# Performance work log

Measured on AMD Instinct MI355X. Metric: run time of the kernel, lower is better.

The kernel has to match this reference:

```python
import jax, jax.numpy as jnp
import numpy as np

N = 100000      # nodes
E = 1600000     # edges (avg degree 16)
F_IN = 128      # dataset.num_features
H = 64          # hidden_channels
C = 40          # dataset.num_classes
LAYERS = 4      # number_conv_layers
EPS = 1e-12     # F.normalize eps


def _agnn_layer(x, src, dst):
    # AGNNConv with beta=1 (requires_grad=False):
    # alpha_ij = softmax_i( cos(x_i, x_j) ), out_i = sum_j alpha_ij * x_j
    xn = x / jnp.maximum(jnp.linalg.norm(x, axis=1, keepdims=True), EPS)
    logits = jnp.sum(xn[dst] * xn[src], axis=1)                      # [E]
    m = jax.lax.stop_gradient(jax.ops.segment_max(logits, dst, num_segments=N))
    e = jnp.exp(logits - m[dst])
    s = jax.ops.segment_sum(e, dst, num_segments=N)
    alpha = e / s[dst]                                               # [E]
    return jax.ops.segment_sum(alpha[:, None] * x[src], dst, num_segments=N)


def setup_inputs() -> dict:
    key = jax.random.key(0)
    k = jax.random.split(key, 6)
    x = jax.random.normal(k[0], (N, F_IN), dtype=jnp.float32)
    edge_index = jax.random.randint(k[1], (2, E), 0, N, dtype=jnp.int32)
    W1 = jax.random.normal(k[2], (F_IN, H), dtype=jnp.float32) * (1.0 / np.sqrt(F_IN))
    b1 = jnp.zeros((H,), dtype=jnp.float32)
    W2 = jax.random.normal(k[3], (H, C), dtype=jnp.float32) * (1.0 / np.sqrt(H))
    b2 = jnp.zeros((C,), dtype=jnp.float32)
    return {"x": x, "W1": W1, "b1": b1, "W2": W2, "b2": b2, "edge_index": edge_index}


def reference(x, W1, b1, W2, b2, edge_index):
    # add self loops (PyG AGNNConv default)
    loop = jnp.arange(N, dtype=edge_index.dtype)
    src = jnp.concatenate([edge_index[0], loop])
    dst = jnp.concatenate([edge_index[1], loop])
    h = jax.nn.relu(x @ W1 + b1)          # lin1 + relu (dropout p=0 / eval)
    for _ in range(LAYERS):
        h = _agnn_layer(h, src, dst)
    out = h @ W2 + b2                     # lin2
    return jax.nn.log_softmax(out, axis=1)
```

## Files before the change

kernel.cpp:

```cpp
#include <hip/hip_runtime.h>
#include <math.h>

#define F_IN 128
#define H_DIM 64
#define C_OUT 40
#define NBK 391
#define CHUNK 4096
#define XPAD 136
#define PHB 128

typedef _Float16 h8 __attribute__((ext_vector_type(8)));
typedef _Float16 half2t __attribute__((ext_vector_type(2)));
typedef float nf4 __attribute__((ext_vector_type(4)));
typedef _Float16 f16x8 __attribute__((ext_vector_type(8)));
typedef float f32x4 __attribute__((ext_vector_type(4)));

union H8 {
    h8 v;
    half2t p[4];
};

__device__ __forceinline__ float dot8(const H8& a, const H8& b) {
    float d = __builtin_amdgcn_fdot2(a.p[0], b.p[0], 0.0f, false);
    d = __builtin_amdgcn_fdot2(a.p[1], b.p[1], d, false);
    d = __builtin_amdgcn_fdot2(a.p[2], b.p[2], d, false);
    d = __builtin_amdgcn_fdot2(a.p[3], b.p[3], d, false);
    return d;
}

__device__ __forceinline__ float dpp_red8_add(float x) {
    int v = __builtin_bit_cast(int, x);
    x += __builtin_bit_cast(float, __builtin_amdgcn_update_dpp(0, v, 0xB1, 0xF, 0xF, true));
    v = __builtin_bit_cast(int, x);
    x += __builtin_bit_cast(float, __builtin_amdgcn_update_dpp(0, v, 0x4E, 0xF, 0xF, true));
    v = __builtin_bit_cast(int, x);
    x += __builtin_bit_cast(float, __builtin_amdgcn_update_dpp(0, v, 0x141, 0xF, 0xF, true));
    return x;
}


__global__ void __launch_bounds__(256) bphist_kernel(const int* __restrict__ dst,
                                                     int* __restrict__ part, int E) {
    __shared__ int lh[512];
    int tid = threadIdx.x;
    lh[tid] = 0; lh[tid + 256] = 0;
    __syncthreads();
    int slice = (E + PHB - 1) / PHB;
    int lo = blockIdx.x * slice;
    int hi = min(E, lo + slice);
    for (int e = lo + tid; e < hi; e += 256) {
        int d = __builtin_nontemporal_load(&dst[e]);
        atomicAdd(&lh[d >> 8], 1);
    }
    __syncthreads();
    part[blockIdx.x * 512 + tid] = lh[tid];
    part[blockIdx.x * 512 + tid + 256] = lh[tid + 256];
}

__global__ void __launch_bounds__(512) bscan_kernel(const int* __restrict__ part,
                                                    int* __restrict__ bbase,
                                                    int* __restrict__ bcursor, int E) {
    __shared__ int sa[512], sb[512];
    int t = threadIdx.x;
    int v = 0;
#pragma unroll 4
    for (int b = 0; b < PHB; b++) v += part[b * 512 + t];
    sa[t] = v;
    __syncthreads();
    int* pa = sa; int* pb = sb;
#pragma unroll
    for (int off = 1; off < 512; off <<= 1) {
        pb[t] = pa[t] + ((t >= off) ? pa[t - off] : 0);
        __syncthreads();
        int* tmp = pa; pa = pb; pb = tmp;
    }
    if (t < NBK) {
        int excl = pa[t] - v;
        bbase[t] = excl;
        bcursor[t] = excl;
    }
    if (t == 0) bbase[NBK] = E;
}

__global__ void __launch_bounds__(256) binscatter_kernel(const int* __restrict__ src,
                                                         const int* __restrict__ dst,
                                                         int* __restrict__ bcursor,
                                                         unsigned int* __restrict__ pairs, int E) {
    __shared__ unsigned int sp[CHUNK];
    __shared__ unsigned short sbof[CHUNK];
    __shared__ int hist[512];
    __shared__ int scanA[512], scanB[512];
    __shared__ int cur[512];
    __shared__ int gbase[512];
    int tid = threadIdx.x;
    int e0 = blockIdx.x * CHUNK;
    int cnt = min(CHUNK, E - e0);

    int dv[CHUNK / 256], sv[CHUNK / 256];
#pragma unroll
    for (int i = 0; i < CHUNK / 256; i++) {
        int idx = tid + i * 256;
        if (idx < cnt) {
            dv[i] = __builtin_nontemporal_load(&dst[e0 + idx]);
            sv[i] = __builtin_nontemporal_load(&src[e0 + idx]);
        }
    }
    hist[tid] = 0; hist[tid + 256] = 0;
    __syncthreads();
#pragma unroll
    for (int i = 0; i < CHUNK / 256; i++) {
        int idx = tid + i * 256;
        if (idx < cnt) atomicAdd(&hist[dv[i] >> 8], 1);
    }
    __syncthreads();
    scanA[tid] = hist[tid]; scanA[tid + 256] = hist[tid + 256];
    __syncthreads();
    int* pa = scanA; int* pb = scanB;
#pragma unroll
    for (int off = 1; off < 512; off <<= 1) {
        pb[tid] = pa[tid] + ((tid >= off) ? pa[tid - off] : 0);
        int t1 = tid + 256;
        pb[t1] = pa[t1] + ((t1 >= off) ? pa[t1 - off] : 0);
        __syncthreads();
        int* tmp = pa; pa = pb; pb = tmp;
    }
    cur[tid] = pa[tid] - hist[tid];
    cur[tid + 256] = pa[tid + 256] - hist[tid + 256];
    __syncthreads();
#pragma unroll
    for (int i = 0; i < CHUNK / 256; i++) {
        int idx = tid + i * 256;
        if (idx < cnt) {
            int b = dv[i] >> 8;
            int lp = atomicAdd(&cur[b], 1);
            sp[lp] = ((unsigned int)(dv[i] & 255) << 24) | (unsigned int)sv[i];
            sbof[lp] = (unsigned short)b;
        }
    }
    {
        int c0 = hist[tid];
        gbase[tid] = c0 ? atomicAdd(&bcursor[tid], c0) : 0;
        int c1 = hist[tid + 256];
        gbase[tid + 256] = c1 ? atomicAdd(&bcursor[tid + 256], c1) : 0;
    }
    __syncthreads();
    for (int i = tid; i < cnt; i += 256) {
        int b = sbof[i];
        int off_in_b = i - (pa[b] - hist[b]);
        pairs[gbase[b] + off_in_b] = sp[i];
    }
}

__global__ void __launch_bounds__(256) bucketsort_kernel(const unsigned int* __restrict__ pairs,
                                                         const int* __restrict__ bbase,
                                                         int* __restrict__ rowptr,
                                                         int* __restrict__ ssrc, int N, int E) {
    __shared__ int hist[256], scanA[256], scanB[256], cur[256];
    int b = blockIdx.x;
    int tid = threadIdx.x;
    int e0 = bbase[b], e1 = bbase[b + 1];
    hist[tid] = 0;
    __syncthreads();
    for (int e = e0 + tid; e < e1; e += 256) {
        unsigned int p = pairs[e];
        atomicAdd(&hist[p >> 24], 1);
    }
    __syncthreads();
    scanA[tid] = hist[tid];
    __syncthreads();
    int* pa = scanA; int* pb = scanB;
#pragma unroll
    for (int off = 1; off < 256; off <<= 1) {
        pb[tid] = pa[tid] + ((tid >= off) ? pa[tid - off] : 0);
        __syncthreads();
        int* tmp = pa; pa = pb; pb = tmp;
    }
    int excl = pa[tid] - hist[tid];
    int node = (b << 8) + tid;
    if (node < N) rowptr[node] = e0 + excl;
    if (b == NBK - 1 && tid == 0) rowptr[N] = E;
    cur[tid] = e0 + excl;
    __syncthreads();
    for (int e = e0 + tid; e < e1; e += 256) {
        unsigned int p = pairs[e];
        int pos = atomicAdd(&cur[p >> 24], 1);
        ssrc[pos] = (int)(p & 0x00FFFFFFu);
    }
}

__global__ void __launch_bounds__(256) cvtw_kernel(const float* __restrict__ W1,
                                                   _Float16* __restrict__ w1t) {
    int t = blockIdx.x * 256 + threadIdx.x;
    if (t < F_IN * H_DIM) {
        int k = t >> 6, col = t & 63;
        w1t[col * F_IN + k] = (_Float16)W1[t];
    }
}

__global__ void __launch_bounds__(256) lin1_kernel(
        const float* __restrict__ x, const _Float16* __restrict__ w1t,
        const float* __restrict__ b1, _Float16* __restrict__ hnout,
        float* __restrict__ nrmout, int n) {
    __shared__ _Float16 sx[64 * XPAD];
    __shared__ _Float16 sw[64 * XPAD];
    int tid = threadIdx.x;
    int r0 = blockIdx.x * 64;

    for (int ch = tid; ch < 64 * 32; ch += 256) {
        int row = ch >> 5, k4 = (ch & 31) << 2;
        float4 xv = make_float4(0.f, 0.f, 0.f, 0.f);
        if (r0 + row < n) xv = *(const float4*)(x + (size_t)(r0 + row) * F_IN + k4);
        _Float16* p = &sx[row * XPAD + k4];
        p[0] = (_Float16)xv.x; p[1] = (_Float16)xv.y;
        p[2] = (_Float16)xv.z; p[3] = (_Float16)xv.w;
    }
    for (int ch = tid; ch < 64 * 16; ch += 256) {
        int col = ch >> 4, k8 = (ch & 15) << 3;
        *(uint4*)&sw[col * XPAD + k8] = *(const uint4*)(w1t + col * F_IN + k8);
    }
    __syncthreads();

    int w = tid >> 6, lane = tid & 63;
    int q = lane >> 4, c = lane & 15;

    f16x8 afrag[4];
#pragma unroll
    for (int kk = 0; kk < 4; kk++)
        afrag[kk] = *(const f16x8*)&sx[(w * 16 + c) * XPAD + kk * 32 + q * 8];

    f32x4 acc[4] = {{0.f,0.f,0.f,0.f},{0.f,0.f,0.f,0.f},{0.f,0.f,0.f,0.f},{0.f,0.f,0.f,0.f}};
#pragma unroll
    for (int ct = 0; ct < 4; ct++) {
#pragma unroll
        for (int kk = 0; kk < 4; kk++) {
            f16x8 bfrag = *(const f16x8*)&sw[(ct * 16 + c) * XPAD + kk * 32 + q * 8];
            acc[ct] = __builtin_amdgcn_mfma_f32_16x16x32_f16(afrag[kk], bfrag, acc[ct], 0, 0, 0);
        }
    }

    float ss[4] = {0.f, 0.f, 0.f, 0.f};
#pragma unroll
    for (int ct = 0; ct < 4; ct++) {
        float bv = b1[ct * 16 + c];
#pragma unroll
        for (int r = 0; r < 4; r++) {
            float v = fmaxf(acc[ct][r] + bv, 0.0f);
            acc[ct][r] = v;
            ss[r] = fmaf(v, v, ss[r]);
        }
    }
#pragma unroll
    for (int k = 1; k < 16; k <<= 1) {
#pragma unroll
        for (int r = 0; r < 4; r++) ss[r] += __shfl_xor(ss[r], k, 64);
    }
    float nn[4], inv[4];
#pragma unroll
    for (int r = 0; r < 4; r++) {
        nn[r] = fmaxf(sqrtf(ss[r]), 1e-12f);
        inv[r] = 1.0f / nn[r];
    }
#pragma unroll
    for (int ct = 0; ct < 4; ct++)
#pragma unroll
        for (int r = 0; r < 4; r++)
            sx[(w * 16 + q * 4 + r) * XPAD + ct * 16 + c] = (_Float16)(acc[ct][r] * inv[r]);

    if (c == 0) {
#pragma unroll
        for (int r = 0; r < 4; r++) {
            int row = r0 + w * 16 + q * 4 + r;
            if (row < n) nrmout[row] = nn[r];
        }
    }
#pragma unroll
    for (int it = 0; it < 2; it++) {
        int row = w * 16 + it * 8 + (lane >> 3);
        int k8 = (lane & 7) * 8;
        if (r0 + row < n)
            *(uint4*)(hnout + (size_t)(r0 + row) * H_DIM + k8) =
                *(const uint4*)&sx[row * XPAD + k8];
    }
}

__global__ void __launch_bounds__(256, 4) agnn_kernel(
        const h8* __restrict__ h, const float* __restrict__ nrm,
        const int* __restrict__ rowptr, const int* __restrict__ ssrc,
        h8* __restrict__ hout, float* __restrict__ nrmout, int n, int E) {
    int wv = (blockIdx.x * blockDim.x + threadIdx.x) >> 6;
    int lane = threadIdx.x & 63;
    int g = lane >> 3;
    int sub = lane & 7;
    int wid = wv * 8 + g;
    bool nvalid = wid < n;
    int nid = nvalid ? wid : (n - 1);

    int e0 = rowptr[nid];
    int e1 = rowptr[nid + 1];
    int steps = nvalid ? (e1 - e0) : 0;

    H8 hd; hd.v = h[(size_t)nid * 8 + sub];
    float ni = nrm[nid];

    int mx = steps;
    mx = max(mx, __shfl_xor(mx, 8, 64));
    mx = max(mx, __shfl_xor(mx, 16, 64));
    mx = max(mx, __shfl_xor(mx, 32, 64));

    float dself = dpp_red8_add(dot8(hd, hd));
    float wself = __expf(dself);
    float sw = wself;
    float aself = wself * ni;
    half2t ap = {(_Float16)aself, (_Float16)aself};
    half2t acc2[4];
#pragma unroll
    for (int j = 0; j < 4; j++) acc2[j] = ap * hd.p[j];

    for (int it = 0; it < mx; it += 8) {
        int s[8];
#pragma unroll
        for (int k = 0; k < 8; k++) {
            int e = e0 + it + k;
            s[k] = ssrc[min(e, E - 1)];
        }
        H8 X[8];
        float xn[8];
#pragma unroll
        for (int k = 0; k < 8; k++) {
            X[k].v = h[(size_t)s[k] * 8 + sub];
            xn[k] = nrm[s[k]];
        }

        float d[8];
#pragma unroll
        for (int k = 0; k < 8; k++) d[k] = dpp_red8_add(dot8(X[k], hd));
        float w[8];
#pragma unroll
        for (int k = 0; k < 8; k++) w[k] = (it + k < steps) ? __expf(d[k]) : 0.0f;
#pragma unroll
        for (int k = 0; k < 8; k++) sw += w[k];
#pragma unroll
        for (int k = 0; k < 8; k++) {
            float a = w[k] * xn[k];
            half2t apk = {(_Float16)a, (_Float16)a};
#pragma unroll
            for (int j = 0; j < 4; j++) acc2[j] += apk * X[k].p[j];
        }
    }

    float inv = 1.0f / sw;
    float o[8];
#pragma unroll
    for (int j = 0; j < 4; j++) {
        o[2 * j] = (float)acc2[j][0] * inv;
        o[2 * j + 1] = (float)acc2[j][1] * inv;
    }
    float ss = 0.0f;
#pragma unroll
    for (int i = 0; i < 8; i++) ss = fmaf(o[i], o[i], ss);
    ss = dpp_red8_add(ss);
    float nn = fmaxf(sqrtf(ss), 1e-12f);
    float r = 1.0f / nn;
    h8 oh;
#pragma unroll
    for (int i = 0; i < 8; i++) oh[i] = (_Float16)(o[i] * r);
    if (nvalid) {
        hout[(size_t)wid * 8 + sub] = oh;
        if (sub == 0) nrmout[wid] = nn;
    }
}

__global__ void __launch_bounds__(256) lin2_kernel(
        const h8* __restrict__ h, const float* __restrict__ nrm,
        const float* __restrict__ W2, const float* __restrict__ b2,
        float* __restrict__ out, int n) {
    __shared__ h8 sh[32 * 8];
    __shared__ float snrm[32];
    int tid = threadIdx.x;
    int r0 = blockIdx.x * 32;
    int rows = min(32, n - r0);

    {
        const uint4* hg = (const uint4*)(h + (size_t)r0 * 8);
        uint4* sh4 = (uint4*)sh;
        int tot = rows * 8;
        for (int i = tid; i < tot; i += 256) sh4[i] = hg[i];
        if (tid < rows) snrm[tid] = nrm[r0 + tid];
    }
    __syncthreads();

    int wave = tid >> 6, lane = tid & 63;
    int rbase = wave * 8;

    float acc[8];
    if (lane < C_OUT) {
#pragma unroll
        for (int j = 0; j < 8; j++) acc[j] = 0.0f;
#pragma unroll 2
        for (int k = 0; k < H_DIM; k += 8) {
            float w[8];
#pragma unroll
            for (int i = 0; i < 8; i++) w[i] = W2[(k + i) * C_OUT + lane];
#pragma unroll
            for (int j = 0; j < 8; j++) {
                h8 hv = sh[(rbase + j) * 8 + (k >> 3)];
#pragma unroll
                for (int i = 0; i < 8; i++) acc[j] = fmaf((float)hv[i], w[i], acc[j]);
            }
        }
        float bl = b2[lane];
#pragma unroll
        for (int j = 0; j < 8; j++) acc[j] = fmaf(snrm[rbase + j], acc[j], bl);
    } else {
#pragma unroll
        for (int j = 0; j < 8; j++) acc[j] = -INFINITY;
    }

#pragma unroll
    for (int j = 0; j < 8; j++) {
        int r = rbase + j;
        if (r >= rows) break;
        float m = acc[j];
#pragma unroll
        for (int k = 1; k < 64; k <<= 1) m = fmaxf(m, __shfl_xor(m, k, 64));
        float e = (lane < C_OUT) ? __expf(acc[j] - m) : 0.0f;
        float s = e;
#pragma unroll
        for (int k = 1; k < 64; k <<= 1) s += __shfl_xor(s, k, 64);
        if (lane < C_OUT) out[(size_t)(r0 + r) * C_OUT + lane] = acc[j] - m - logf(s);
    }
}


extern "C" void kernel_launch(void* const* d_in, const int* in_sizes, int n_in,
                              void* d_out, int out_size, void* d_ws, size_t ws_size,
                              hipStream_t stream) {
    const float* x = (const float*)d_in[0];
    const float* W1 = (const float*)d_in[1];
    const float* b1 = (const float*)d_in[2];
    const float* W2 = (const float*)d_in[3];
    const float* b2 = (const float*)d_in[4];
    const int* ei = (const int*)d_in[5];

    const int N = in_sizes[0] / F_IN;
    const int E = in_sizes[5] / 2;
    const int* src = ei;
    const int* dst = ei + E;

    char* w = (char*)d_ws;
    auto carve = [&](size_t bytes) {
        char* p = w;
        w += (bytes + 255) & ~(size_t)255;
        return p;
    };
    _Float16* g1 = (_Float16*)carve((size_t)N * H_DIM * 2);
    _Float16* g2 = (_Float16*)carve((size_t)N * H_DIM * 2);
    float* rn1 = (float*)carve((size_t)N * 4);
    float* rn2 = (float*)carve((size_t)N * 4);
    int* rowptr = (int*)carve((size_t)(N + 1) * 4);
    int* bbase = (int*)carve(512 * 4);
    int* bcursor = (int*)carve(512 * 4);
    int* ssrc = (int*)carve((size_t)E * 4);
    _Float16* w1t = (_Float16*)carve((size_t)F_IN * H_DIM * 2);
    unsigned int* pairs = (unsigned int*)g2;
    int* part = (int*)g1;

    bphist_kernel<<<PHB, 256, 0, stream>>>(dst, part, E);
    bscan_kernel<<<1, 512, 0, stream>>>(part, bbase, bcursor, E);
    binscatter_kernel<<<(E + CHUNK - 1) / CHUNK, 256, 0, stream>>>(src, dst, bcursor, pairs, E);
    bucketsort_kernel<<<NBK, 256, 0, stream>>>(pairs, bbase, rowptr, ssrc, N, E);

    cvtw_kernel<<<(F_IN * H_DIM + 255) / 256, 256, 0, stream>>>(W1, w1t);
    lin1_kernel<<<(N + 63) / 64, 256, 0, stream>>>(x, w1t, b1, g1, rn1, N);

    {
        int blocks = (N + 31) / 32;
        agnn_kernel<<<blocks, 256, 0, stream>>>((const h8*)g1, rn1, rowptr, ssrc, (h8*)g2, rn2, N, E);
        agnn_kernel<<<blocks, 256, 0, stream>>>((const h8*)g2, rn2, rowptr, ssrc, (h8*)g1, rn1, N, E);
        agnn_kernel<<<blocks, 256, 0, stream>>>((const h8*)g1, rn1, rowptr, ssrc, (h8*)g2, rn2, N, E);
        agnn_kernel<<<blocks, 256, 0, stream>>>((const h8*)g2, rn2, rowptr, ssrc, (h8*)g1, rn1, N, E);
    }

    lin2_kernel<<<(N + 31) / 32, 256, 0, stream>>>((const h8*)g1, rn1, W2, b2, (float*)d_out, N);
}
```

Baseline: 284.6 us.

## Software-pipeline neighbor gathers with double-buffered index and feature loads

Restructures the edge loop in the AGNN aggregation kernel into a two-stage software pipeline. While one batch of 8 neighbors is being computed, the next batch's features and the following batch's indices are already in flight, which is meant to hide gather latency. Edge indices are now clamped to the node's own edge range, so padded lanes stay local. The cost is roughly double the register use for the X buffers, which could reduce occupancy under the 256x4 launch bound, plus extra prefetch loads past the end of each row.

Result: no change. 287.8 us (+1.1%).

```diff
diff --git a/kernel.cpp b/kernel.cpp
--- a/kernel.cpp
+++ b/kernel.cpp
@@ -298,6 +298,7 @@
     int e0 = rowptr[nid];
     int e1 = rowptr[nid + 1];
     int steps = nvalid ? (e1 - e0) : 0;
+    int eclamp = min(max(e1 - 1, e0), E - 1);
 
     H8 hd; hd.v = h[(size_t)nid * 8 + sub];
     float ni = nrm[nid];
@@ -316,36 +317,46 @@
 #pragma unroll
     for (int j = 0; j < 4; j++) acc2[j] = ap * hd.p[j];
 
-    for (int it = 0; it < mx; it += 8) {
-        int s[8];
-#pragma unroll
-        for (int k = 0; k < 8; k++) {
-            int e = e0 + it + k;
-            s[k] = ssrc[min(e, E - 1)];
-        }
-        H8 X[8];
-        float xn[8];
+    int sA[8], sB[8];
+    H8 XA[8], XB[8];
+    float nA[8], nB[8];
+
+    auto SLOAD = [&](int* s, int ofs) {
+#pragma unroll
+        for (int k = 0; k < 8; k++) s[k] = ssrc[min(e0 + ofs + k, eclamp)];
+    };
+    auto HLOAD = [&](const int* s, H8* X, float* xn) {
 #pragma unroll
         for (int k = 0; k < 8; k++) {
             X[k].v = h[(size_t)s[k] * 8 + sub];
             xn[k] = nrm[s[k]];
         }
-
+    };
+    auto COMP = [&](const H8* X, const float* xn, int base) {
         float d[8];
 #pragma unroll
         for (int k = 0; k < 8; k++) d[k] = dpp_red8_add(dot8(X[k], hd));
-        float w[8];
-#pragma unroll
-        for (int k = 0; k < 8; k++) w[k] = (it + k < steps) ? __expf(d[k]) : 0.0f;
-#pragma unroll
-        for (int k = 0; k < 8; k++) sw += w[k];
 #pragma unroll
         for (int k = 0; k < 8; k++) {
-            float a = w[k] * xn[k];
+            float wgt = (base + k < steps) ? __expf(d[k]) : 0.0f;
+            sw += wgt;
+            float a = wgt * xn[k];
             half2t apk = {(_Float16)a, (_Float16)a};
 #pragma unroll
             for (int j = 0; j < 4; j++) acc2[j] += apk * X[k].p[j];
         }
+    };
+
+    SLOAD(sA, 0);
+    HLOAD(sA, XA, nA);
+    SLOAD(sB, 8);
+    for (int it = 0; it < mx; it += 16) {
+        HLOAD(sB, XB, nB);
+        SLOAD(sA, it + 16);
+        COMP(XA, nA, it);
+        HLOAD(sA, XA, nA);
+        SLOAD(sB, it + 24);
+        COMP(XB, nB, it + 8);
     }
 
     float inv = 1.0f / sw;
```
